# Kernel optimization log

Measured on AMD Instinct MI355X. Metric: run time of the kernel, lower is better.

Reference implementation:

```python
import jax, jax.numpy as jnp
import numpy as np

B, TXT_T, MEL_T, N_MEL = 32, 256, 1600, 40
PAD_MAG = 1.0e12


def setup_inputs() -> dict:
    key = jax.random.key(0)
    k1, k2, k3, k4 = jax.random.split(key, 4)
    mu_logvar = jax.random.normal(k1, (B, TXT_T, 2 * N_MEL), jnp.float32)
    z = jax.random.normal(k2, (B, N_MEL, MEL_T), jnp.float32)
    text_lengths = jax.random.randint(k3, (B,), TXT_T // 2, TXT_T + 1).astype(jnp.int32)
    mel_lengths = jax.random.randint(k4, (B,), MEL_T // 2, MEL_T + 1).astype(jnp.int32)
    return {"mu_logvar": mu_logvar, "z": z,
            "text_lengths": text_lengths, "mel_lengths": mel_lengths}


def _mdn_log_prob(mu_logvar, z):
    # mu_logvar: [B, L, 2C], z: [B, C, T] -> log_prob_matrix [B, L, T]
    C = z.shape[1]
    mu, logvar = jnp.split(mu_logvar, 2, axis=-1)          # [B, L, C] each
    invvar = jnp.exp(-logvar)                               # [B, L, C]
    # mean_c((z - mu)^2 * invvar) expanded via matmuls (no [B,L,T,C] tensor)
    t1 = jnp.einsum('bct,blc->blt', z * z, invvar)
    t2 = jnp.einsum('bct,blc->blt', z, mu * invvar)
    t3 = jnp.sum(mu * mu * invvar, axis=-1)[:, :, None]
    mse = t1 - 2.0 * t2 + t3                                # [B, L, T]
    return -0.5 * (mse / C + jnp.mean(logvar, axis=-1)[:, :, None])


def _forward_dp(lp):
    # forward algorithm: log_alpha over (txt position, mel time) via scan over T
    Bb, L, T = lp.shape
    alpha0 = jnp.full((Bb, L + 1), -PAD_MAG, lp.dtype).at[:, 1].set(lp[:, 0, 0])

    def step(alpha, lp_t):
        stay = alpha[:, 1:] + 1e-7
        go = alpha[:, :-1] + 1e-7
        new = jnp.logaddexp(stay, go) + lp_t                # [B, L]
        alpha_new = jnp.concatenate(
            [jnp.full((Bb, 1), -PAD_MAG, lp.dtype), new], axis=1)
        return alpha_new, new

    _, ys = jax.lax.scan(step, alpha0, jnp.moveaxis(lp[:, :, 1:], 2, 0))
    log_alpha = jnp.concatenate([alpha0[:, 1:][None], ys], axis=0)  # [T, B, L]
    return log_alpha


def _viterbi(lp, text_lengths, mel_lengths):
    Bb, L, T = lp.shape
    beta0 = jnp.full((Bb, L), -PAD_MAG, lp.dtype).at[:, 0].set(lp[:, 0, 0])

    def fstep(beta, lp_t):
        shifted = jnp.concatenate(
            [jnp.full((Bb, 1), -PAD_MAG, lp.dtype), beta[:, :-1]], axis=1)
        new = jnp.maximum(beta, shifted) + lp_t
        return new, new

    _, ys = jax.lax.scan(fstep, beta0, jnp.moveaxis(lp[:, :, 1:], 2, 0))
    log_beta = jnp.transpose(jnp.concatenate([beta0[None], ys], axis=0), (1, 2, 0))  # [B, L, T]

    b_idx = jnp.arange(Bb)
    r0 = (text_lengths - 1).astype(jnp.float32)
    c0 = (mel_lengths - 1).astype(jnp.float32)

    def bstep(carry, _):
        rows, cols = carry
        ri = rows.astype(jnp.int32)
        ci = cols.astype(jnp.int32)
        # torch negative indexing wraps -> emulate with mod
        val_go = log_beta[b_idx, (ri - 1) % L, (ci - 1) % T]
        val_stay = log_beta[b_idx, ri % L, (ci - 1) % T]
        is_go = (val_go > val_stay).astype(rows.dtype)
        new_rows = jax.nn.relu(rows - is_go + 1.0) - 1.0
        new_cols = jax.nn.relu(cols) - 1.0
        return (new_rows, new_cols), new_rows

    _, path_ys = jax.lax.scan(bstep, (r0, c0), None, length=T - 1)
    full = jnp.concatenate([r0[None], path_ys], axis=0)     # [T, B], backward order
    path = full[::-1].T                                     # [B, T], chronological
    align = jax.nn.one_hot(path.astype(jnp.int32), L, dtype=lp.dtype)  # [B, T, L]

    def shift(a, ml):
        # F.pad(..., (-pad, pad)) on time axis: shift valid region to the front
        rolled = jnp.roll(a, -(T - ml), axis=0)
        mask = (jnp.arange(T) < ml)[:, None].astype(a.dtype)
        return rolled * mask

    return jax.vmap(shift)(align, mel_lengths)              # [B, T, L]


def reference(mu_logvar, z, text_lengths, mel_lengths):
    lp = _mdn_log_prob(mu_logvar, z)                        # [B, L, T]
    log_alpha = _forward_dp(lp)                             # [T, B, L]
    b_idx = jnp.arange(lp.shape[0])
    alpha_last = log_alpha[mel_lengths - 1, b_idx, text_lengths - 1]
    mdn_loss = -(alpha_last / mel_lengths.astype(alpha_last.dtype))  # [B]
    alignment = _viterbi(lp, text_lengths, mel_lengths)     # [B, T, L]
    return mdn_loss, alignment, lp
```

## Files before the change

### kernel.cpp

```cpp
#include <hip/hip_runtime.h>
#include <cstdint>
#include <math.h>

#define BB   32
#define LLEN 256
#define TLEN 1600
#define NC   40
#define NEGPADF (-1.0e12f)
#define NEGPADD (-1.0e12)

#define LOG2E_F 1.4426950408889634f
#define LN2_F   0.6931471805599453f
#define C7F     1.4426950408889634e-7f

#define OFF_ALIGN 32
#define OFF_LP    (32 + (size_t)BB * TLEN * LLEN)

#define WSB_A    0
#define WSB_KC   (WSB_A + (size_t)BB * LLEN * 80 * 8)
#define WSB_LPT  (WSB_KC + (size_t)BB * LLEN * 8)

__device__ __forceinline__ int imin(int a, int b) { return a < b ? a : b; }

#define WAIT_LGKM0 0xC07F
#define WAIT_VM0   0x3F70

__device__ __forceinline__ int rot1_i32(int x) {
  return __builtin_amdgcn_mov_dpp(x, 0x13C , 0xF, 0xF, true);
}
__device__ __forceinline__ float rot1_f32(float x) {
  return __int_as_float(rot1_i32(__float_as_int(x)));
}
__device__ __forceinline__ double rot1_f64(double x) {
  long long v = __double_as_longlong(x);
  int lo = rot1_i32((int)(v & 0xffffffffLL));
  int hi = rot1_i32((int)(v >> 32));
  return __longlong_as_double(((long long)hi << 32) | (unsigned long long)(unsigned int)lo);
}

__global__ __launch_bounds__(256) void prep_kernel(
    const float* __restrict__ mu_logvar, double* __restrict__ A, double* __restrict__ Kc) {
  int row = blockIdx.x * 4 + (threadIdx.x >> 6);
  int lane = threadIdx.x & 63;
  const float* src = mu_logvar + (size_t)row * (2 * NC);
  double mu = 0.0, lv = 0.0, iv = 0.0, part = 0.0;
  if (lane < NC) {
    mu = (double)src[lane];
    lv = (double)src[NC + lane];
    iv = exp(-lv);
    part = mu * mu * iv + lv;
  }
  for (int m = 1; m < 64; m <<= 1) part += __shfl_xor(part, m, 64);
  const double s = -0.5 / (double)NC;
  if (lane < NC) {
    A[(size_t)row * 80 + lane]      = s * iv;
    A[(size_t)row * 80 + NC + lane] = (1.0 / (double)NC) * mu * iv;
  }
  if (lane == 0) Kc[row] = s * part;
}

__global__ __launch_bounds__(128) void lp_kernel(
    const float* __restrict__ z, const double* __restrict__ A,
    const double* __restrict__ Kc, float* __restrict__ out,
    float* __restrict__ lpTh) {
  int b  = blockIdx.z;
  int l0 = blockIdx.y * 32;
  int t0 = blockIdx.x * 128;
  int tid = threadIdx.x;
  int t = t0 + tid;
  int tv = imin(t, TLEN - 1);
  bool act = (t < TLEN);

  float* lp_out = out + OFF_LP;
  float* loS    = out + OFF_ALIGN;

  float zr[NC];
  const float* zb = z + (size_t)b * NC * TLEN;
  #pragma unroll
  for (int c = 0; c < NC; ++c) zr[c] = zb[(size_t)c * TLEN + tv];

  __shared__ __align__(16) double tile[128][17];
  const double* Ab = A + ((size_t)b * LLEN + l0) * 80;
  const double* Kb = Kc + (size_t)b * LLEN + l0;

  for (int g = 0; g < 2; ++g) {
    for (int j16 = 0; j16 < 16; ++j16) {
      int j = g * 16 + j16;
      const double* Ar = Ab + (size_t)j * 80;
      double a0 = Kb[j], a1 = 0.0, a2 = 0.0, a3 = 0.0;
      #pragma unroll
      for (int c = 0; c < NC; c += 2) {
        double z0 = (double)zr[c], z1 = (double)zr[c + 1];
        a0 = fma(Ar[c],          z0 * z0, a0);
        a1 = fma(Ar[NC + c],     z0,      a1);
        a2 = fma(Ar[c + 1],      z1 * z1, a2);
        a3 = fma(Ar[NC + c + 1], z1,      a3);
      }
      double accd = (a0 + a2) + (a1 + a3);
      if (act) lp_out[((size_t)b * LLEN + l0 + j) * TLEN + t] = (float)accd;
      tile[tid][j16] = accd;
    }
    __syncthreads();
    #pragma unroll
    for (int p = 0; p < 4; ++p) {
      int idx = p * 128 + tid;
      int r = idx >> 2, c4 = idx & 3;
      int tr = t0 + r;
      if (tr < TLEN) {
        float h[4], lo[4];
        #pragma unroll
        for (int i = 0; i < 4; ++i) {
          double d = tile[r][c4 * 4 + i];
          float hh = (float)d;
          h[i] = hh;
          lo[i] = (float)(d - (double)hh);
        }
        size_t base = ((size_t)b * TLEN + tr) * LLEN + l0 + g * 16 + c4 * 4;
        *(float4*)(lpTh + base) = make_float4(h[0], h[1], h[2], h[3]);
        *(float4*)(loS + base)  = make_float4(lo[0], lo[1], lo[2], lo[3]);
      }
    }
    __syncthreads();
  }
}

__global__ __launch_bounds__(64, 1) void dp_kernel(
    const float* __restrict__ lpTh, const float* outR,
    const int* __restrict__ tlen, const int* __restrict__ mlen,
    float* out) {
  int bid = blockIdx.x;
  bool is_beta = (bid >= BB);
  int b = is_beta ? bid - BB : bid;
  int lane = threadIdx.x & 63;
  int tl = tlen[b];
  int ml = mlen[b];
  const float* lpb = lpTh + (size_t)b * TLEN * LLEN;
  const float* lob = outR + OFF_ALIGN + (size_t)b * TLEN * LLEN;
  float* al = out + OFF_ALIGN + (size_t)b * TLEN * LLEN;

  __shared__ uint32_t Dbits[LLEN][TLEN / 32];
  __shared__ int pathL[TLEN];

  const float* ph = lpb + 4 * lane;

  if (!is_beta) {
    float lp00 = lpb[0] * LOG2E_F;
    float o0 = (lane == 0) ? lp00 : NEGPADF;
    float o1 = NEGPADF, o2 = NEGPADF, o3 = NEGPADF;
    float f0 = o0, f1 = o1, f2 = o2, f3 = o3;
    float qv = rot1_f32(o3);
    float4 h0 = *(const float4*)(ph + 1 * LLEN);
    float4 h1 = *(const float4*)(ph + 2 * LLEN);
    float4 h2 = *(const float4*)(ph + 3 * LLEN);
    float4 h3 = *(const float4*)(ph + 4 * LLEN);
    float4 h4 = *(const float4*)(ph + 5 * LLEN);
    float4 h5 = *(const float4*)(ph + 6 * LLEN);
    float4 h6 = *(const float4*)(ph + 7 * LLEN);
    float4 h7 = *(const float4*)(ph + 8 * LLEN);
    int t = 1;
    auto stepA = [&](float4& hs) {
      float4 hv = hs;
      int c = imin(t + 8, TLEN - 1);
      hs = *(const float4*)(ph + (size_t)c * LLEN);
      float l0 = fmaf(hv.x, LOG2E_F, C7F);
      float l1 = fmaf(hv.y, LOG2E_F, C7F);
      float l2 = fmaf(hv.z, LOG2E_F, C7F);
      float l3 = fmaf(hv.w, LOG2E_F, C7F);
      float p = (lane == 0) ? NEGPADF : qv;
      float m0 = fmaxf(o0, p),  d0 = o0 - p;
      float m1 = fmaxf(o1, o0), d1 = o1 - o0;
      float m2 = fmaxf(o2, o1), d2 = o2 - o1;
      float m3 = fmaxf(o3, o2), d3 = o3 - o2;
      float n0 = m0 + __builtin_amdgcn_logf(1.0f + __builtin_amdgcn_exp2f(-fabsf(d0))) + l0;
      float n1 = m1 + __builtin_amdgcn_logf(1.0f + __builtin_amdgcn_exp2f(-fabsf(d1))) + l1;
      float n2 = m2 + __builtin_amdgcn_logf(1.0f + __builtin_amdgcn_exp2f(-fabsf(d2))) + l2;
      float n3 = m3 + __builtin_amdgcn_logf(1.0f + __builtin_amdgcn_exp2f(-fabsf(d3))) + l3;
      o0 = n0; o1 = n1; o2 = n2; o3 = n3;
      qv = rot1_f32(o3);
      if (t == ml - 1) { f0 = o0; f1 = o1; f2 = o2; f3 = o3; }
      ++t;
    };
    for (int tb = 0; tb < TLEN / 8; ++tb) {
      stepA(h0); stepA(h1); stepA(h2); stepA(h3);
      stepA(h4); stepA(h5); stepA(h6); stepA(h7);
    }
    int fr = tl - 1;
    if (lane == (fr >> 2)) {
      int sx = fr & 3;
      float val = (sx == 0) ? f0 : (sx == 1) ? f1 : (sx == 2) ? f2 : f3;
      out[b] = -val * LN2_F / (float)ml;
    }
    return;
  }

  const float* pl = lob + 4 * lane;
  float* az = al + 4 * lane;
  float4 z4 = make_float4(0.f, 0.f, 0.f, 0.f);
  double lp00 = (double)lpb[0] + (double)lob[0];
  double o0 = (lane == 0) ? lp00 : NEGPADD;
  double o1 = NEGPADD, o2 = NEGPADD, o3 = NEGPADD;
  uint32_t a0 = 0, a1 = (lane == 0) ? 1u : 0u, a2 = 0, a3 = 0;
  double qv = rot1_f64(o3);
  float4 h0 = *(const float4*)(ph + 1 * LLEN), g0 = *(const float4*)(pl + 1 * LLEN);
  float4 h1 = *(const float4*)(ph + 2 * LLEN), g1 = *(const float4*)(pl + 2 * LLEN);
  float4 h2 = *(const float4*)(ph + 3 * LLEN), g2 = *(const float4*)(pl + 3 * LLEN);
  float4 h3 = *(const float4*)(ph + 4 * LLEN), g3 = *(const float4*)(pl + 4 * LLEN);
  float4 h4 = *(const float4*)(ph + 5 * LLEN), g4 = *(const float4*)(pl + 5 * LLEN);
  float4 h5 = *(const float4*)(ph + 6 * LLEN), g5 = *(const float4*)(pl + 6 * LLEN);
  float4 h6 = *(const float4*)(ph + 7 * LLEN), g6 = *(const float4*)(pl + 7 * LLEN);
  float4 h7 = *(const float4*)(ph + 8 * LLEN), g7 = *(const float4*)(pl + 8 * LLEN);
  int t = 1;
  auto stepB = [&](float4& hs, float4& gs) {
    float4 hv = hs; float4 gv = gs;
    int c = imin(t + 8, TLEN - 1);
    hs = *(const float4*)(ph + (size_t)c * LLEN);
    gs = *(const float4*)(pl + (size_t)c * LLEN);
    double l0 = (double)hv.x + (double)gv.x;
    double l1 = (double)hv.y + (double)gv.y;
    double l2 = (double)hv.z + (double)gv.z;
    double l3 = (double)hv.w + (double)gv.w;
    double p = (lane == 0) ? NEGPADD : qv;
    double n0 = fmax(o0, p)  + l0;
    double n1 = fmax(o1, o0) + l1;
    double n2 = fmax(o2, o1) + l2;
    double n3 = fmax(o3, o2) + l3;
    qv = rot1_f64(n3);
    uint32_t bit = 1u << (t & 31);
    if (qv > n0) a0 |= bit;
    if (n0 > n1) a1 |= bit;
    if (n1 > n2) a2 |= bit;
    if (n2 > n3) a3 |= bit;
    o0 = n0; o1 = n1; o2 = n2; o3 = n3;
    if ((t & 31) == 31) {
      int wd = t >> 5;
      Dbits[4 * lane + 0][wd] = a0; a0 = 0;
      Dbits[4 * lane + 1][wd] = a1; a1 = 0;
      Dbits[4 * lane + 2][wd] = a2; a2 = 0;
      Dbits[4 * lane + 3][wd] = a3; a3 = 0;
    }
    if (t > 8) *(float4*)(az + (size_t)(t - 8) * LLEN) = z4;
    ++t;
  };
  for (int tb = 0; tb < TLEN / 8; ++tb) {
    stepB(h0, g0); stepB(h1, g1); stepB(h2, g2); stepB(h3, g3);
    stepB(h4, g4); stepB(h5, g5); stepB(h6, g6); stepB(h7, g7);
  }
  *(float4*)az = z4;
  #pragma unroll
  for (int c = TLEN - 7; c < TLEN; ++c)
    *(float4*)(az + (size_t)c * LLEN) = z4;

  __builtin_amdgcn_s_waitcnt(WAIT_LGKM0);

  if (lane == 0) {
    int r = tl - 1;
    pathL[ml - 1] = r;
    int curR = 1 << 30, curW = -1;
    uint32_t W = 0;
    for (int qq = ml - 2; qq >= 0; --qq) {
      int w2 = qq >> 5;
      if (r >= 0 && (r != curR || w2 != curW)) { W = Dbits[r][w2]; curR = r; curW = w2; }
      int g = (r >= 0) ? (int)((W >> (qq & 31)) & 1u) : 0;
      r -= g;
      pathL[qq] = r;
    }
  }
  __builtin_amdgcn_s_waitcnt(WAIT_LGKM0);
  __builtin_amdgcn_s_waitcnt(WAIT_VM0);

  for (int tt = lane; tt < ml; tt += 64) {
    int p = pathL[tt];
    if (p >= 0) al[(size_t)tt * LLEN + p] = 1.0f;
  }
}

extern "C" void kernel_launch(void* const* d_in, const int* in_sizes, int n_in,
                              void* d_out, int out_size, void* d_ws, size_t ws_size,
                              hipStream_t stream) {
  const float* mu_logvar = (const float*)d_in[0];
  const float* z         = (const float*)d_in[1];
  const int*   tlv       = (const int*)d_in[2];
  const int*   mlv       = (const int*)d_in[3];
  float* out = (float*)d_out;
  char*  wsb = (char*)d_ws;

  double* Ad   = (double*)(wsb + WSB_A);
  double* Kcd  = (double*)(wsb + WSB_KC);
  float*  lpTh = (float*)(wsb + WSB_LPT);

  prep_kernel<<<dim3(BB * LLEN / 4), 256, 0, stream>>>(mu_logvar, Ad, Kcd);
  lp_kernel<<<dim3(13, 8, BB), 128, 0, stream>>>(z, Ad, Kcd, out, lpTh);
  dp_kernel<<<dim3(2 * BB), 64, 0, stream>>>(lpTh, out, tlv, mlv, out);
}
```

Measured before the change: 549.9 us.

## Store lp as split doubles, polynomial softplus, shift-based viterbi bit packing

The lp kernel now writes exact double values into two interleaved double2 buffers instead of float hi/lo pairs, so the Viterbi pass loads doubles directly without reconstructing them. The forward pass replaces log(1+exp2(-d)) with a cubic polynomial in exp2(-d), shortening the serial dependency chain per step, and reads half its inputs from the row-major lp output. Viterbi decision bits are accumulated with v_cmp plus add-with-carry shifts, which reverses the bit order, and the backtrack indexing is adjusted to match. The risks are polynomial approximation error in the loss and uncoalesced strided loads in the forward pass.

```diff
diff --git a/kernel.cpp b/kernel.cpp
--- a/kernel.cpp
+++ b/kernel.cpp
@@ -12,6 +12,9 @@
 #define LOG2E_F 1.4426950408889634f
 #define LN2_F   0.6931471805599453f
 #define C7F     1.4426950408889634e-7f
+#define PA_F 1.4426950f
+#define PB_F (-0.6484000f)
+#define PC_F 0.2057000f
 
 #define OFF_ALIGN 32
 #define OFF_LP    (32 + (size_t)BB * TLEN * LLEN)
@@ -61,7 +64,7 @@
 
 __global__ __launch_bounds__(128) void lp_kernel(
     const float* __restrict__ z, const double* __restrict__ A,
-    const double* __restrict__ Kc, float* __restrict__ out,
+    const double* __restrict__ Kc, float* out,
     float* __restrict__ lpTh) {
   int b  = blockIdx.z;
   int l0 = blockIdx.y * 32;
@@ -72,7 +75,8 @@
   bool act = (t < TLEN);
 
   float* lp_out = out + OFF_LP;
-  float* loS    = out + OFF_ALIGN;
+  double2* bufA = (double2*)lpTh;
+  double2* bufB = (double2*)(out + OFF_ALIGN);
 
   float zr[NC];
   const float* zb = z + (size_t)b * NC * TLEN;
@@ -107,17 +111,12 @@
       int r = idx >> 2, c4 = idx & 3;
       int tr = t0 + r;
       if (tr < TLEN) {
-        float h[4], lo[4];
-        #pragma unroll
-        for (int i = 0; i < 4; ++i) {
-          double d = tile[r][c4 * 4 + i];
-          float hh = (float)d;
-          h[i] = hh;
-          lo[i] = (float)(d - (double)hh);
-        }
-        size_t base = ((size_t)b * TLEN + tr) * LLEN + l0 + g * 16 + c4 * 4;
-        *(float4*)(lpTh + base) = make_float4(h[0], h[1], h[2], h[3]);
-        *(float4*)(loS + base)  = make_float4(lo[0], lo[1], lo[2], lo[3]);
+        size_t chunk = ((size_t)b * TLEN + tr) * 64 + (l0 + g * 16) / 4 + c4;
+        double2 dA, dB;
+        dA.x = tile[r][c4 * 4 + 0]; dA.y = tile[r][c4 * 4 + 1];
+        dB.x = tile[r][c4 * 4 + 2]; dB.y = tile[r][c4 * 4 + 3];
+        bufA[chunk] = dA;
+        bufB[chunk] = dB;
       }
     }
     __syncthreads();
@@ -134,55 +133,72 @@
   int lane = threadIdx.x & 63;
   int tl = tlen[b];
   int ml = mlen[b];
-  const float* lpb = lpTh + (size_t)b * TLEN * LLEN;
-  const float* lob = outR + OFF_ALIGN + (size_t)b * TLEN * LLEN;
+  const double2* pA = (const double2*)lpTh + (size_t)b * TLEN * 64;
+  const double2* pB = (const double2*)(outR + OFF_ALIGN) + (size_t)b * TLEN * 64;
   float* al = out + OFF_ALIGN + (size_t)b * TLEN * LLEN;
 
   __shared__ uint32_t Dbits[LLEN][TLEN / 32];
   __shared__ int pathL[TLEN];
 
-  const float* ph = lpb + 4 * lane;
-
   if (!is_beta) {
-    float lp00 = lpb[0] * LOG2E_F;
+    const float* gB = outR + OFF_LP + (size_t)b * LLEN * TLEN;
+    int off2 = (4 * lane + 2) * TLEN;
+    int off3 = off2 + TLEN;
+    double2 v00 = pA[lane];
+    float lp00 = (float)v00.x * LOG2E_F;
     float o0 = (lane == 0) ? lp00 : NEGPADF;
     float o1 = NEGPADF, o2 = NEGPADF, o3 = NEGPADF;
     float f0 = o0, f1 = o1, f2 = o2, f3 = o3;
     float qv = rot1_f32(o3);
-    float4 h0 = *(const float4*)(ph + 1 * LLEN);
-    float4 h1 = *(const float4*)(ph + 2 * LLEN);
-    float4 h2 = *(const float4*)(ph + 3 * LLEN);
-    float4 h3 = *(const float4*)(ph + 4 * LLEN);
-    float4 h4 = *(const float4*)(ph + 5 * LLEN);
-    float4 h5 = *(const float4*)(ph + 6 * LLEN);
-    float4 h6 = *(const float4*)(ph + 7 * LLEN);
-    float4 h7 = *(const float4*)(ph + 8 * LLEN);
+    double2 hA0, hA1, hA2, hA3, hA4, hA5, hA6, hA7;
+    float r20, r21, r22, r23, r24, r25, r26, r27;
+    float r30, r31, r32, r33, r34, r35, r36, r37;
+    hA0 = pA[1 * 64 + lane]; { const float* bt = gB + 1; r20 = bt[off2]; r30 = bt[off3]; }
+    hA1 = pA[2 * 64 + lane]; { const float* bt = gB + 2; r21 = bt[off2]; r31 = bt[off3]; }
+    hA2 = pA[3 * 64 + lane]; { const float* bt = gB + 3; r22 = bt[off2]; r32 = bt[off3]; }
+    hA3 = pA[4 * 64 + lane]; { const float* bt = gB + 4; r23 = bt[off2]; r33 = bt[off3]; }
+    hA4 = pA[5 * 64 + lane]; { const float* bt = gB + 5; r24 = bt[off2]; r34 = bt[off3]; }
+    hA5 = pA[6 * 64 + lane]; { const float* bt = gB + 6; r25 = bt[off2]; r35 = bt[off3]; }
+    hA6 = pA[7 * 64 + lane]; { const float* bt = gB + 7; r26 = bt[off2]; r36 = bt[off3]; }
+    hA7 = pA[8 * 64 + lane]; { const float* bt = gB + 8; r27 = bt[off2]; r37 = bt[off3]; }
     int t = 1;
-    auto stepA = [&](float4& hs) {
-      float4 hv = hs;
+    auto stepA = [&](double2& ha, float& r2, float& r3) {
+      float v0 = (float)ha.x, v1 = (float)ha.y;
+      float v2 = r2, v3 = r3;
       int c = imin(t + 8, TLEN - 1);
-      hs = *(const float4*)(ph + (size_t)c * LLEN);
-      float l0 = fmaf(hv.x, LOG2E_F, C7F);
-      float l1 = fmaf(hv.y, LOG2E_F, C7F);
-      float l2 = fmaf(hv.z, LOG2E_F, C7F);
-      float l3 = fmaf(hv.w, LOG2E_F, C7F);
+      ha = (pA + (size_t)c * 64)[lane];
+      { const float* bt = gB + c; r2 = bt[off2]; r3 = bt[off3]; }
+      float l0 = fmaf(v0, LOG2E_F, C7F);
+      float l1 = fmaf(v1, LOG2E_F, C7F);
+      float l2 = fmaf(v2, LOG2E_F, C7F);
+      float l3 = fmaf(v3, LOG2E_F, C7F);
       float p = (lane == 0) ? NEGPADF : qv;
-      float m0 = fmaxf(o0, p),  d0 = o0 - p;
-      float m1 = fmaxf(o1, o0), d1 = o1 - o0;
-      float m2 = fmaxf(o2, o1), d2 = o2 - o1;
-      float m3 = fmaxf(o3, o2), d3 = o3 - o2;
-      float n0 = m0 + __builtin_amdgcn_logf(1.0f + __builtin_amdgcn_exp2f(-fabsf(d0))) + l0;
-      float n1 = m1 + __builtin_amdgcn_logf(1.0f + __builtin_amdgcn_exp2f(-fabsf(d1))) + l1;
-      float n2 = m2 + __builtin_amdgcn_logf(1.0f + __builtin_amdgcn_exp2f(-fabsf(d2))) + l2;
-      float n3 = m3 + __builtin_amdgcn_logf(1.0f + __builtin_amdgcn_exp2f(-fabsf(d3))) + l3;
+      float m0 = fmaxf(o0, p),  d0 = fabsf(o0 - p);
+      float m1 = fmaxf(o1, o0), d1 = fabsf(o1 - o0);
+      float m2 = fmaxf(o2, o1), d2 = fabsf(o2 - o1);
+      float m3 = fmaxf(o3, o2), d3 = fabsf(o3 - o2);
+      float y0 = __builtin_amdgcn_exp2f(-d0);
+      float y1 = __builtin_amdgcn_exp2f(-d1);
+      float y2 = __builtin_amdgcn_exp2f(-d2);
+      float y3 = __builtin_amdgcn_exp2f(-d3);
+      float s0 = y0 * fmaf(y0, fmaf(y0, PC_F, PB_F), PA_F);
+      float s1 = y1 * fmaf(y1, fmaf(y1, PC_F, PB_F), PA_F);
+      float s2 = y2 * fmaf(y2, fmaf(y2, PC_F, PB_F), PA_F);
+      float s3 = y3 * fmaf(y3, fmaf(y3, PC_F, PB_F), PA_F);
+      float n0 = m0 + s0 + l0;
+      float n1 = m1 + s1 + l1;
+      float n2 = m2 + s2 + l2;
+      float n3 = m3 + s3 + l3;
       o0 = n0; o1 = n1; o2 = n2; o3 = n3;
       qv = rot1_f32(o3);
       if (t == ml - 1) { f0 = o0; f1 = o1; f2 = o2; f3 = o3; }
       ++t;
     };
     for (int tb = 0; tb < TLEN / 8; ++tb) {
-      stepA(h0); stepA(h1); stepA(h2); stepA(h3);
-      stepA(h4); stepA(h5); stepA(h6); stepA(h7);
+      stepA(hA0, r20, r30); stepA(hA1, r21, r31);
+      stepA(hA2, r22, r32); stepA(hA3, r23, r33);
+      stepA(hA4, r24, r34); stepA(hA5, r25, r35);
+      stepA(hA6, r26, r36); stepA(hA7, r27, r37);
     }
     int fr = tl - 1;
     if (lane == (fr >> 2)) {
@@ -193,43 +209,45 @@
     return;
   }
 
-  const float* pl = lob + 4 * lane;
-  float* az = al + 4 * lane;
   float4 z4 = make_float4(0.f, 0.f, 0.f, 0.f);
-  double lp00 = (double)lpb[0] + (double)lob[0];
+  double2 v00 = pA[lane];
+  double lp00 = v00.x;
   double o0 = (lane == 0) ? lp00 : NEGPADD;
   double o1 = NEGPADD, o2 = NEGPADD, o3 = NEGPADD;
   uint32_t a0 = 0, a1 = (lane == 0) ? 1u : 0u, a2 = 0, a3 = 0;
   double qv = rot1_f64(o3);
-  float4 h0 = *(const float4*)(ph + 1 * LLEN), g0 = *(const float4*)(pl + 1 * LLEN);
-  float4 h1 = *(const float4*)(ph + 2 * LLEN), g1 = *(const float4*)(pl + 2 * LLEN);
-  float4 h2 = *(const float4*)(ph + 3 * LLEN), g2 = *(const float4*)(pl + 3 * LLEN);
-  float4 h3 = *(const float4*)(ph + 4 * LLEN), g3 = *(const float4*)(pl + 4 * LLEN);
-  float4 h4 = *(const float4*)(ph + 5 * LLEN), g4 = *(const float4*)(pl + 5 * LLEN);
-  float4 h5 = *(const float4*)(ph + 6 * LLEN), g5 = *(const float4*)(pl + 6 * LLEN);
-  float4 h6 = *(const float4*)(ph + 7 * LLEN), g6 = *(const float4*)(pl + 7 * LLEN);
-  float4 h7 = *(const float4*)(ph + 8 * LLEN), g7 = *(const float4*)(pl + 8 * LLEN);
+  double2 hA0 = pA[1 * 64 + lane], hB0 = pB[1 * 64 + lane];
+  double2 hA1 = pA[2 * 64 + lane], hB1 = pB[2 * 64 + lane];
+  double2 hA2 = pA[3 * 64 + lane], hB2 = pB[3 * 64 + lane];
+  double2 hA3 = pA[4 * 64 + lane], hB3 = pB[4 * 64 + lane];
+  double2 hA4 = pA[5 * 64 + lane], hB4 = pB[5 * 64 + lane];
+  double2 hA5 = pA[6 * 64 + lane], hB5 = pB[6 * 64 + lane];
+  double2 hA6 = pA[7 * 64 + lane], hB6 = pB[7 * 64 + lane];
+  double2 hA7 = pA[8 * 64 + lane], hB7 = pB[8 * 64 + lane];
   int t = 1;
-  auto stepB = [&](float4& hs, float4& gs) {
-    float4 hv = hs; float4 gv = gs;
+  auto stepB = [&](double2& ha, double2& hb) {
+    double l0 = ha.x, l1 = ha.y, l2 = hb.x, l3 = hb.y;
     int c = imin(t + 8, TLEN - 1);
-    hs = *(const float4*)(ph + (size_t)c * LLEN);
-    gs = *(const float4*)(pl + (size_t)c * LLEN);
-    double l0 = (double)hv.x + (double)gv.x;
-    double l1 = (double)hv.y + (double)gv.y;
-    double l2 = (double)hv.z + (double)gv.z;
-    double l3 = (double)hv.w + (double)gv.w;
+    ha = (pA + (size_t)c * 64)[lane];
+    hb = (pB + (size_t)c * 64)[lane];
     double p = (lane == 0) ? NEGPADD : qv;
     double n0 = fmax(o0, p)  + l0;
     double n1 = fmax(o1, o0) + l1;
     double n2 = fmax(o2, o1) + l2;
     double n3 = fmax(o3, o2) + l3;
     qv = rot1_f64(n3);
-    uint32_t bit = 1u << (t & 31);
-    if (qv > n0) a0 |= bit;
-    if (n0 > n1) a1 |= bit;
-    if (n1 > n2) a2 |= bit;
-    if (n2 > n3) a3 |= bit;
+    asm("v_cmp_gt_f64 vcc, %1, %2\n\t"
+        "v_addc_co_u32 %0, vcc, %0, %0, vcc"
+        : "+v"(a0) : "v"(qv), "v"(n0) : "vcc");
+    asm("v_cmp_gt_f64 vcc, %1, %2\n\t"
+        "v_addc_co_u32 %0, vcc, %0, %0, vcc"
+        : "+v"(a1) : "v"(n0), "v"(n1) : "vcc");
+    asm("v_cmp_gt_f64 vcc, %1, %2\n\t"
+        "v_addc_co_u32 %0, vcc, %0, %0, vcc"
+        : "+v"(a2) : "v"(n1), "v"(n2) : "vcc");
+    asm("v_cmp_gt_f64 vcc, %1, %2\n\t"
+        "v_addc_co_u32 %0, vcc, %0, %0, vcc"
+        : "+v"(a3) : "v"(n2), "v"(n3) : "vcc");
     o0 = n0; o1 = n1; o2 = n2; o3 = n3;
     if ((t & 31) == 31) {
       int wd = t >> 5;
@@ -238,17 +256,17 @@
       Dbits[4 * lane + 2][wd] = a2; a2 = 0;
       Dbits[4 * lane + 3][wd] = a3; a3 = 0;
     }
-    if (t > 8) *(float4*)(az + (size_t)(t - 8) * LLEN) = z4;
+    if (t > 8) ((float4*)(al + (size_t)(t - 8) * LLEN))[lane] = z4;
     ++t;
   };
   for (int tb = 0; tb < TLEN / 8; ++tb) {
-    stepB(h0, g0); stepB(h1, g1); stepB(h2, g2); stepB(h3, g3);
-    stepB(h4, g4); stepB(h5, g5); stepB(h6, g6); stepB(h7, g7);
-  }
-  *(float4*)az = z4;
+    stepB(hA0, hB0); stepB(hA1, hB1); stepB(hA2, hB2); stepB(hA3, hB3);
+    stepB(hA4, hB4); stepB(hA5, hB5); stepB(hA6, hB6); stepB(hA7, hB7);
+  }
+  ((float4*)al)[lane] = z4;
   #pragma unroll
   for (int c = TLEN - 7; c < TLEN; ++c)
-    *(float4*)(az + (size_t)c * LLEN) = z4;
+    ((float4*)(al + (size_t)c * LLEN))[lane] = z4;
 
   __builtin_amdgcn_s_waitcnt(WAIT_LGKM0);
 
@@ -260,7 +278,7 @@
     for (int qq = ml - 2; qq >= 0; --qq) {
       int w2 = qq >> 5;
       if (r >= 0 && (r != curR || w2 != curW)) { W = Dbits[r][w2]; curR = r; curW = w2; }
-      int g = (r >= 0) ? (int)((W >> (qq & 31)) & 1u) : 0;
+      int g = (r >= 0) ? (int)((W >> (31 - (qq & 31))) & 1u) : 0;
       r -= g;
       pathL[qq] = r;
     }
```

Result: faster. 527.3 us (-4.1%).
